# Kernel tuning notes

Measured on AMD Instinct MI355X. Metric: run time of the kernel, lower is better.

Reference implementation:

```python
import jax, jax.numpy as jnp
import numpy as np

N_NODES = 20000
N_EDGES = 50000
IN_DIM = 128
HID = 128
OUT_DIM = 64
N_PAIRS = 128
N_LAYERS = 2
N_HEADS = 4


def setup_inputs() -> dict:
    key = jax.random.key(0)
    ks = jax.random.split(key, 32)
    s = 0.05
    def p(k, shape):
        return jax.random.normal(k, shape, jnp.float32) * s
    inp = {}
    inp["node_features"] = jax.random.normal(ks[0], (N_NODES, IN_DIM), jnp.float32)
    inp["edge_index"] = jax.random.randint(ks[1], (2, N_EDGES), 0, N_NODES, jnp.int32)
    inp["edge_timestamps"] = jax.random.uniform(ks[2], (N_EDGES,), jnp.float32)
    inp["target_pairs"] = jax.random.randint(ks[3], (N_PAIRS, 2), 0, N_NODES, jnp.int32)
    inp["in_W"] = p(ks[4], (HID, IN_DIM)); inp["in_b"] = p(ks[5], (HID,))
    inp["te_W1"] = p(ks[6], (N_LAYERS, HID, 1)); inp["te_b1"] = p(ks[7], (N_LAYERS, HID))
    inp["te_W2"] = p(ks[8], (N_LAYERS, HID, HID)); inp["te_b2"] = p(ks[9], (N_LAYERS, HID))
    inp["attn_in_W"] = p(ks[10], (N_LAYERS, 3 * HID, HID)); inp["attn_in_b"] = p(ks[11], (N_LAYERS, 3 * HID))
    inp["attn_out_W"] = p(ks[12], (N_LAYERS, HID, HID)); inp["attn_out_b"] = p(ks[13], (N_LAYERS, HID))
    inp["ft_W"] = p(ks[14], (N_LAYERS, HID, HID)); inp["ft_b"] = p(ks[15], (N_LAYERS, HID))
    inp["op_W"] = p(ks[16], (N_LAYERS, HID, HID)); inp["op_b"] = p(ks[17], (N_LAYERS, HID))
    inp["out1_W"] = p(ks[18], (HID, HID)); inp["out1_b"] = p(ks[19], (HID,))
    inp["out2_W"] = p(ks[20], (OUT_DIM, HID)); inp["out2_b"] = p(ks[21], (OUT_DIM,))
    inp["lp1_W"] = p(ks[22], (HID, 2 * OUT_DIM)); inp["lp1_b"] = p(ks[23], (HID,))
    inp["lp2_W"] = p(ks[24], (HID // 2, HID)); inp["lp2_b"] = p(ks[25], (HID // 2,))
    inp["lp3_W"] = p(ks[26], (1, HID // 2)); inp["lp3_b"] = p(ks[27], (1,))
    return inp


def _forward(node_features, edge_index, edge_timestamps, target_pairs,
             in_W, in_b, te_W1, te_b1, te_W2, te_b2,
             attn_in_W, attn_in_b, attn_out_W, attn_out_b,
             ft_W, ft_b, op_W, op_b,
             out1_W, out1_b, out2_W, out2_b,
             lp1_W, lp1_b, lp2_W, lp2_b, lp3_W, lp3_b):
    N = node_features.shape[0]
    h = in_W.shape[0]
    H = N_HEADS
    d = h // H
    scale = 1.0 / np.sqrt(d).astype(np.float32)
    src, dst = edge_index[0], edge_index[1]
    # flattened target nodes; duplicates compute identical rows so dedup (torch.unique) is unneeded
    targets = target_pairs.reshape(-1)  # [U]
    U = targets.shape[0]
    E = src.shape[0]

    x = node_features @ in_W.T + in_b  # [N, h]
    for l in range(te_W1.shape[0]):
        tf = x @ ft_W[l].T + ft_b[l]                                           # [N, h]
        tfeat = jax.nn.relu(edge_timestamps[:, None] @ te_W1[l].T + te_b1[l])
        tfeat = tfeat @ te_W2[l].T + te_b2[l]                                  # [E, h]
        Wq, Wk, Wv = jnp.split(attn_in_W[l], 3, axis=0)
        bq, bk, bv = jnp.split(attn_in_b[l], 3)
        q = (tf[targets] @ Wq.T + bq).reshape(U, H, d)
        # keys/values are linear in (tf[nbr] + tfeat): split into node term A and edge term B
        Ak = (tf @ Wk.T).reshape(N, H, d)
        Bk = (tfeat @ Wk.T + bk).reshape(E, H, d)
        Av = (tf @ Wv.T).reshape(N, H, d)
        Bv = (tfeat @ Wv.T + bv).reshape(E, H, d)
        is_src = src[None, :] == targets[:, None]          # [U, E]
        mask = is_src | (dst[None, :] == targets[:, None])  # edge incident to target
        nbr = jnp.where(is_src, dst[None, :], src[None, :])  # other endpoint, [U, E]
        qAk = jnp.einsum('uhd,nhd->uhn', q, Ak) * scale      # [U, H, N]
        idx = jnp.broadcast_to(nbr[:, None, :], (U, H, E))
        s_node = jnp.take_along_axis(qAk, idx, axis=2)        # [U, H, E]
        s_edge = jnp.einsum('uhd,ehd->uhe', q, Bk) * scale
        scores = jnp.where(mask[:, None, :], s_node + s_edge, -1e30)
        p = jax.nn.softmax(scores, axis=-1)
        p = jnp.where(mask[:, None, :], p, 0.0)               # [U, H, E]
        out_edge = jnp.einsum('uhe,ehd->uhd', p, Bv)
        # sum_e p * Av[nbr] via per-target scatter of probs into node space
        w = jax.vmap(lambda pe, ne: jax.ops.segment_sum(pe, ne, num_segments=N))(
            p.transpose(0, 2, 1), nbr)                        # [U, N, H]
        out_node = jnp.einsum('unh,nhd->uhd', w, Av)
        attn = (out_node + out_edge).reshape(U, h) @ attn_out_W[l].T + attn_out_b[l]
        has_nbr = mask.any(axis=1)
        agg_in = jnp.where(has_nbr[:, None], attn, tf[targets])
        agg = agg_in @ op_W[l].T + op_b[l]
        x = x.at[targets].set(agg)
        x = jax.nn.relu(x)
    emb = jax.nn.relu(x @ out1_W.T + out1_b) @ out2_W.T + out2_b  # [N, out]
    pair = jnp.concatenate([emb[target_pairs[:, 0]], emb[target_pairs[:, 1]]], axis=1)
    z = jax.nn.relu(pair @ lp1_W.T + lp1_b)
    z = jax.nn.relu(z @ lp2_W.T + lp2_b)
    return jax.nn.sigmoid(z @ lp3_W.T + lp3_b)  # [B, 1]


def reference(node_features, edge_index, edge_timestamps, target_pairs,
              in_W, in_b, te_W1, te_b1, te_W2, te_b2,
              attn_in_W, attn_in_b, attn_out_W, attn_out_b,
              ft_W, ft_b, op_W, op_b,
              out1_W, out1_b, out2_W, out2_b,
              lp1_W, lp1_b, lp2_W, lp2_b, lp3_W, lp3_b):
    return _forward(node_features, edge_index, edge_timestamps, target_pairs,
                    in_W, in_b, te_W1, te_b1, te_W2, te_b2,
                    attn_in_W, attn_in_b, attn_out_W, attn_out_b,
                    ft_W, ft_b, op_W, op_b,
                    out1_W, out1_b, out2_W, out2_b,
                    lp1_W, lp1_b, lp2_W, lp2_b, lp3_W, lp3_b)
```

## Files before the change

kernel.cpp:

```cpp
#include <hip/hip_runtime.h>
#include <math.h>

#define N_NODES 20000
#define N_EDGES 50000
#define N_SLOTS 256
#define N_PAIRS 128
#define CAP 32
#define MSTRIDE 16384
#define NMAT 19
#define TFLAG (1 << 30)
#define HSZ 1024
#define NBLK 256

__device__ __forceinline__ float4 relu4(float4 v) {
    return make_float4(fmaxf(v.x, 0.f), fmaxf(v.y, 0.f), fmaxf(v.z, 0.f), fmaxf(v.w, 0.f));
}
__device__ __forceinline__ float4 add4(float4 a, float4 b) {
    return make_float4(a.x + b.x, a.y + b.y, a.z + b.z, a.w + b.w);
}
__device__ __forceinline__ void fma4(float4& acc, const float4 w, const float s) {
    acc.x = fmaf(w.x, s, acc.x); acc.y = fmaf(w.y, s, acc.y);
    acc.z = fmaf(w.z, s, acc.z); acc.w = fmaf(w.w, s, acc.w);
}
#define F4Z make_float4(0.f, 0.f, 0.f, 0.f)

__device__ __forceinline__ void gbar(unsigned* cnt, unsigned target, bool wait) {
    __syncthreads();
    if (threadIdx.x == 0) {
        __builtin_amdgcn_fence(__ATOMIC_RELEASE, "agent");
        __hip_atomic_fetch_add(cnt, 1u, __ATOMIC_RELAXED, __HIP_MEMORY_SCOPE_AGENT);
        if (wait) {
            int it = 0;
            while (true) {
                unsigned v;
                if ((it++ & 7) != 7)
                    v = __hip_atomic_load(cnt, __ATOMIC_RELAXED,
                                          __HIP_MEMORY_SCOPE_SYSTEM);
                else
                    v = __hip_atomic_fetch_add(cnt, 0u, __ATOMIC_RELAXED,
                                               __HIP_MEMORY_SCOPE_AGENT);
                if (v >= target) break;
                __builtin_amdgcn_s_sleep(16);
            }
            __builtin_amdgcn_fence(__ATOMIC_ACQUIRE, "agent");
        }
    }
    __syncthreads();
}

__device__ __forceinline__ float4 mv_ks1_g8(const float* __restrict__ WT,
                                            const float* __restrict__ xv128,
                                            int g, int jj) {
    const float4* W4 = (const float4*)WT;
    const float4* x4 = (const float4*)xv128;
    float4 acc = F4Z;
#pragma unroll
    for (int kk4 = 0; kk4 < 4; ++kk4) {
        int k4 = g * 4 + kk4;
        float4 xv = x4[k4];
        fma4(acc, W4[(k4 * 4 + 0) * 32 + jj], xv.x);
        fma4(acc, W4[(k4 * 4 + 1) * 32 + jj], xv.y);
        fma4(acc, W4[(k4 * 4 + 2) * 32 + jj], xv.z);
        fma4(acc, W4[(k4 * 4 + 3) * 32 + jj], xv.w);
    }
    return acc;
}
__device__ __forceinline__ float4 mv_ks1_g8_64(const float* __restrict__ WT,
                                               const float* __restrict__ xv128,
                                               int g, int jj) {
    const float4* W4 = (const float4*)WT;
    const float4* x4 = (const float4*)xv128;
    int j16 = jj & 15;
    float4 acc = F4Z;
#pragma unroll
    for (int kk4 = 0; kk4 < 4; ++kk4) {
        int k4 = g * 4 + kk4;
        float4 xv = x4[k4];
        fma4(acc, W4[(k4 * 4 + 0) * 16 + j16], xv.x);
        fma4(acc, W4[(k4 * 4 + 1) * 16 + j16], xv.y);
        fma4(acc, W4[(k4 * 4 + 2) * 16 + j16], xv.z);
        fma4(acc, W4[(k4 * 4 + 3) * 16 + j16], xv.w);
    }
    return acc;
}
__device__ __forceinline__ void mv8_g8(const float* __restrict__ WT,
                                       const float* __restrict__ xs,
                                       int g, int jj, float4* acc) {
    const float4* W4 = (const float4*)WT;
    const float4* x4 = (const float4*)xs;
#pragma unroll
    for (int kk4 = 0; kk4 < 4; ++kk4) {
        int k4 = g * 4 + kk4;
        float4 w0 = W4[(k4 * 4 + 0) * 32 + jj];
        float4 w1 = W4[(k4 * 4 + 1) * 32 + jj];
        float4 w2 = W4[(k4 * 4 + 2) * 32 + jj];
        float4 w3 = W4[(k4 * 4 + 3) * 32 + jj];
#pragma unroll
        for (int e = 0; e < 8; ++e) {
            float4 xv = x4[e * 32 + k4];
            fma4(acc[e], w0, xv.x); fma4(acc[e], w1, xv.y);
            fma4(acc[e], w2, xv.z); fma4(acc[e], w3, xv.w);
        }
    }
}
__device__ __forceinline__ float4 comb1_g8(const float4* pb, int jj) {
    float4 s = pb[jj];
#pragma unroll
    for (int gp = 1; gp < 8; ++gp) s = add4(s, pb[gp * 32 + jj]);
    return s;
}
__device__ __forceinline__ float4 comb8_g8(const float4* pb, int it, int jj) {
    float4 s = pb[it * 32 + jj];
#pragma unroll
    for (int gp = 1; gp < 8; ++gp) s = add4(s, pb[(gp * 8 + it) * 32 + jj]);
    return s;
}

__device__ __forceinline__ float4 mv_ks1(const float* __restrict__ WT,
                                         const float* __restrict__ xv128,
                                         int g, int jj) {
    const float4* W4 = (const float4*)WT;
    const float4* x4 = (const float4*)xv128;
    float4 acc = F4Z;
#pragma unroll 2
    for (int kk4 = 0; kk4 < 8; ++kk4) {
        int k4 = g * 8 + kk4;
        float4 xv = x4[k4];
        fma4(acc, W4[(k4 * 4 + 0) * 32 + jj], xv.x);
        fma4(acc, W4[(k4 * 4 + 1) * 32 + jj], xv.y);
        fma4(acc, W4[(k4 * 4 + 2) * 32 + jj], xv.z);
        fma4(acc, W4[(k4 * 4 + 3) * 32 + jj], xv.w);
    }
    return acc;
}
__device__ __forceinline__ float4 mv_ks1_64(const float* __restrict__ WT,
                                            const float* __restrict__ xv128,
                                            int g, int jj) {
    const float4* W4 = (const float4*)WT;
    const float4* x4 = (const float4*)xv128;
    int j16 = jj & 15;
    float4 acc = F4Z;
#pragma unroll 2
    for (int kk4 = 0; kk4 < 8; ++kk4) {
        int k4 = g * 8 + kk4;
        float4 xv = x4[k4];
        fma4(acc, W4[(k4 * 4 + 0) * 16 + j16], xv.x);
        fma4(acc, W4[(k4 * 4 + 1) * 16 + j16], xv.y);
        fma4(acc, W4[(k4 * 4 + 2) * 16 + j16], xv.z);
        fma4(acc, W4[(k4 * 4 + 3) * 16 + j16], xv.w);
    }
    return acc;
}
__device__ __forceinline__ float4 comb1(const float4* pb, int jj) {
    return add4(add4(pb[jj], pb[32 + jj]), add4(pb[64 + jj], pb[96 + jj]));
}

__device__ __forceinline__ unsigned thash(int key) {
    return ((unsigned)key * 2654435761u) >> 22;
}
__device__ __forceinline__ bool hexists(const int* __restrict__ hkey, int key) {
    unsigned h = thash(key);
    while (true) {
        int k = hkey[h];
        if (k == -1) return false;
        if (k == key) return true;
        h = (h + 1) & (HSZ - 1);
    }
}
__device__ __forceinline__ void hemit_g(const int* __restrict__ hkey,
                                        const int* __restrict__ hval,
                                        int* __restrict__ gcnt,
                                        int2* __restrict__ lst,
                                        int key, int e, int nbrf) {
    unsigned h = thash(key);
    while (true) {
        int k = hkey[h];
        if (k == -1) return;
        if (k == key) {
            int s = hval[h];
            int pos = atomicAdd(&gcnt[s], 1);
            if (pos < CAP) lst[s * CAP + pos] = make_int2(e, nbrf);
        }
        h = (h + 1) & (HSZ - 1);
    }
}

struct Params {
    const float* nf; const int* ei; const float* ts; const int* tp;
    const float* inW; const float* inb;
    const float* teW1; const float* teb1; const float* teW2; const float* teb2;
    const float* aiW; const float* aib; const float* aoW; const float* aob;
    const float* ftW; const float* ftb; const float* opW; const float* opb;
    const float* o1W; const float* o1b; const float* o2W; const float* o2b;
    const float* l1W; const float* l1b; const float* l2W; const float* l2b;
    const float* l3W; const float* l3b;
    float* out; float* x; int* cnt; int2* lst; float* emb; float* WT;
    unsigned* bar;
};

__global__ __launch_bounds__(256, 1) void k_fused(Params P) {
    __shared__ __align__(16) float xu[128], x0u[128], tfv[128], qv[128], sv[128];
    __shared__ __align__(16) float xs[8 * 128], t1s[8 * 128], x0s[8 * 128], zs[8 * 128];
    __shared__ __align__(16) float4 pb[8 * 8 * 32];
    __shared__ __align__(16) float vbl[CAP * 128];
    __shared__ float scl[CAP * 4];
    __shared__ int nbr_s[8], tf_s[8];
    __shared__ float ts_s[8];
    __shared__ __align__(16) float tile[32][129];
    __shared__ int hkey[HSZ], hval[HSZ];

    const int b = blockIdx.x, tid = threadIdx.x, g = tid >> 5, jj = tid & 31;

    if (b < 72) {
        int m, r0, rows;
        if (b < 68) { m = b >> 2; r0 = (b & 3) * 32; rows = 128; }
        else { int mm = b - 68; m = 17 + (mm >> 1); r0 = (mm & 1) * 32; rows = 64; }
        const float* src;
        if (m == 0) src = P.inW;
        else if (m <= 2) src = P.ftW + (m - 1) * MSTRIDE;
        else if (m <= 4) src = P.teW2 + (m - 3) * MSTRIDE;
        else if (m <= 10) src = P.aiW + (m - 5) * MSTRIDE;
        else if (m <= 12) src = P.aoW + (m - 11) * MSTRIDE;
        else if (m <= 14) src = P.opW + (m - 13) * MSTRIDE;
        else if (m == 15) src = P.o1W;
        else if (m == 16) src = P.l1W;
        else if (m == 17) src = P.o2W;
        else src = P.l2W;
        float* dst = P.WT + m * MSTRIDE;
        for (int idx = tid; idx < 32 * 128; idx += 256) {
            int r = idx >> 7, cc = idx & 127;
            tile[r][cc] = src[(r0 + r) * 128 + cc];
        }
        __syncthreads();
        for (int idx = tid; idx < 128 * 32; idx += 256) {
            int k = idx >> 5, jr = idx & 31;
            dst[k * rows + r0 + jr] = tile[jr][k];
        }
    } else {
        for (int i = tid; i < HSZ; i += 256) hkey[i] = -1;
        __syncthreads();
        {
            int uu = P.tp[tid];
            unsigned h = thash(uu);
            while (atomicCAS(&hkey[h], -1, uu) != -1) h = (h + 1) & (HSZ - 1);
            hval[h] = tid;
        }
        __syncthreads();
        const int4* s4 = (const int4*)P.ei;
        const int4* d4 = (const int4*)(P.ei + N_EDGES);
        const int NE4 = N_EDGES / 4;
        const int nscan = NBLK - 72;
        const int chunk = (NE4 + nscan - 1) / nscan;
        const int start = (b - 72) * chunk;
        const int end = min(start + chunk, NE4);
        for (int e4 = start + tid; e4 < end; e4 += 256) {
            int4 s = s4[e4];
            int4 d = d4[e4];
            int ss[4] = {s.x, s.y, s.z, s.w};
            int dd[4] = {d.x, d.y, d.z, d.w};
#pragma unroll
            for (int t = 0; t < 4; ++t) {
                int a = ss[t], bb = dd[t];
                bool atgt = hexists(hkey, a);
                bool btgt = (bb == a) ? atgt : hexists(hkey, bb);
                if (!atgt && !btgt) continue;
                int e = e4 * 4 + t;
                if (atgt) hemit_g(hkey, hval, P.cnt, P.lst, a, e, bb | (btgt ? TFLAG : 0));
                if (btgt && bb != a) hemit_g(hkey, hval, P.cnt, P.lst, bb, e, a | (atgt ? TFLAG : 0));
            }
        }
    }
    gbar(P.bar, NBLK, true);

    const float scale = 0.17677669529663687f;
    const int u = P.tp[b];
    const int c = min(P.cnt[b], CAP);

    for (int layer = 0; layer < 2; ++layer) {
        const float* WT_in = P.WT;
        const float* WT_ft = P.WT + (1 + layer) * MSTRIDE;
        const float* WT_te2 = P.WT + (3 + layer) * MSTRIDE;
        const float* WT_q = P.WT + (5 + 3 * layer) * MSTRIDE;
        const float* WT_k = P.WT + (6 + 3 * layer) * MSTRIDE;
        const float* WT_v = P.WT + (7 + 3 * layer) * MSTRIDE;
        const float* WT_ao = P.WT + (11 + layer) * MSTRIDE;
        const float* WT_op = P.WT + (13 + layer) * MSTRIDE;
        const float* inb = P.inb;
        const float* ftb = P.ftb + layer * 128;
        const float* teW1 = P.teW1 + layer * 128;
        const float* teb1 = P.teb1 + layer * 128;
        const float* teb2 = P.teb2 + layer * 128;
        const float* bq = P.aib + layer * 384;
        const float* bk = bq + 128;
        const float* bv = bq + 256;
        const float* aob = P.aob + layer * 128;
        const float* opb = P.opb + layer * 128;

        if (tid < 128) xu[tid] = (layer == 0) ? P.nf[(size_t)u * 128 + tid]
                                              : P.x[(size_t)u * 128 + tid];
        __syncthreads();
        const float* xeff = xu;
        if (layer == 0) {
            pb[g * 32 + jj] = mv_ks1_g8(WT_in, xu, g, jj);
            __syncthreads();
            if (g == 0)
                *(float4*)(x0u + jj * 4) = add4(comb1_g8(pb, jj), *(const float4*)(inb + jj * 4));
            xeff = x0u;
            __syncthreads();
        }
        pb[g * 32 + jj] = mv_ks1_g8(WT_ft, xeff, g, jj);
        __syncthreads();
        if (g == 0)
            *(float4*)(tfv + jj * 4) = add4(comb1_g8(pb, jj), *(const float4*)(ftb + jj * 4));
        __syncthreads();
        pb[g * 32 + jj] = mv_ks1_g8(WT_q, tfv, g, jj);
        __syncthreads();
        if (g == 0)
            *(float4*)(qv + jj * 4) = add4(comb1_g8(pb, jj), *(const float4*)(bq + jj * 4));
        __syncthreads();

        for (int base = 0; base < c; base += 8) {
            if (tid < 8) {
                int i = base + tid;
                int2 en = (i < c) ? P.lst[b * CAP + i] : make_int2(0, 0);
                nbr_s[tid] = en.y & ~TFLAG;
                tf_s[tid] = (en.y & TFLAG) ? 1 : 0;
                ts_s[tid] = (i < c) ? P.ts[en.x] : 0.f;
            }
            __syncthreads();
            {
                int e = tid >> 5, c0 = jj * 4;
                const float* srcp = (layer == 0) ? (P.nf + (size_t)nbr_s[e] * 128 + c0)
                                                 : (P.x + (size_t)nbr_s[e] * 128 + c0);
                float4 v = *(const float4*)srcp;
                float* dstp = (layer == 0) ? xs : x0s;
                *(float4*)(dstp + e * 128 + c0) = v;
                float tse = ts_s[e];
                float4 w = *(const float4*)(teW1 + c0);
                float4 bb = *(const float4*)(teb1 + c0);
                *(float4*)(t1s + e * 128 + c0) =
                    make_float4(fmaxf(fmaf(tse, w.x, bb.x), 0.f),
                                fmaxf(fmaf(tse, w.y, bb.y), 0.f),
                                fmaxf(fmaf(tse, w.z, bb.z), 0.f),
                                fmaxf(fmaf(tse, w.w, bb.w), 0.f));
            }
            __syncthreads();
            if (layer == 0) {
                float4 acc[8] = {F4Z, F4Z, F4Z, F4Z, F4Z, F4Z, F4Z, F4Z};
                mv8_g8(WT_in, xs, g, jj, acc);
#pragma unroll
                for (int e = 0; e < 8; ++e) pb[(g * 8 + e) * 32 + jj] = acc[e];
                __syncthreads();
                {
                    float4 x0v = add4(comb8_g8(pb, g, jj), *(const float4*)(inb + jj * 4));
                    *(float4*)(x0s + g * 128 + jj * 4) = x0v;
                    if (base + g < c && !tf_s[g])
                        *(float4*)(P.x + (size_t)nbr_s[g] * 128 + jj * 4) = relu4(x0v);
                }
                __syncthreads();
            }
            {
                float4 acc[8] = {F4Z, F4Z, F4Z, F4Z, F4Z, F4Z, F4Z, F4Z};
                mv8_g8(WT_ft, x0s, g, jj, acc);
#pragma unroll
                for (int e = 0; e < 8; ++e) pb[(g * 8 + e) * 32 + jj] = acc[e];
                __syncthreads();
                float4 za = comb8_g8(pb, g, jj);
                __syncthreads();
                float4 acc2[8] = {F4Z, F4Z, F4Z, F4Z, F4Z, F4Z, F4Z, F4Z};
                mv8_g8(WT_te2, t1s, g, jj, acc2);
#pragma unroll
                for (int e = 0; e < 8; ++e) pb[(g * 8 + e) * 32 + jj] = acc2[e];
                __syncthreads();
                float4 zb = comb8_g8(pb, g, jj);
                float4 z4 = add4(add4(za, zb),
                                 add4(*(const float4*)(ftb + jj * 4),
                                      *(const float4*)(teb2 + jj * 4)));
                *(float4*)(zs + g * 128 + jj * 4) = z4;
                __syncthreads();
            }
            {
                float4 acc[8] = {F4Z, F4Z, F4Z, F4Z, F4Z, F4Z, F4Z, F4Z};
                mv8_g8(WT_k, zs, g, jj, acc);
#pragma unroll
                for (int e = 0; e < 8; ++e) pb[(g * 8 + e) * 32 + jj] = acc[e];
                __syncthreads();
                float4 kk = add4(comb8_g8(pb, g, jj), *(const float4*)(bk + jj * 4));
                __syncthreads();
                float4 acc2[8] = {F4Z, F4Z, F4Z, F4Z, F4Z, F4Z, F4Z, F4Z};
                mv8_g8(WT_v, zs, g, jj, acc2);
#pragma unroll
                for (int e = 0; e < 8; ++e) pb[(g * 8 + e) * 32 + jj] = acc2[e];
                __syncthreads();
                float4 vv = add4(comb8_g8(pb, g, jj), *(const float4*)(bv + jj * 4));
                float4 q4 = *(const float4*)(qv + jj * 4);
                float pr = q4.x * kk.x + q4.y * kk.y + q4.z * kk.z + q4.w * kk.w;
                pr += __shfl_xor(pr, 1);
                pr += __shfl_xor(pr, 2);
                pr += __shfl_xor(pr, 4);
                if (base + g < c) {
                    if ((jj & 7) == 0) scl[(base + g) * 4 + (jj >> 3)] = pr * scale;
                    *(float4*)(vbl + (base + g) * 128 + jj * 4) = vv;
                }
                __syncthreads();
            }
        }

        if (tid < 128) {
            int h = tid >> 5;
            if (c > 0) {
                float m = -INFINITY;
                for (int i = 0; i < c; ++i) m = fmaxf(m, scl[i * 4 + h]);
                float l = 0.f, o = 0.f;
                for (int i = 0; i < c; ++i) {
                    float p = __expf(scl[i * 4 + h] - m);
                    l += p;
                    o = fmaf(p, vbl[i * 128 + tid], o);
                }
                sv[tid] = o / l;
            } else {
                sv[tid] = 0.f;
            }
        }
        __syncthreads();
        pb[g * 32 + jj] = mv_ks1_g8(WT_ao, sv, g, jj);
        __syncthreads();
        if (g == 0) {
            float4 z4;
            if (c > 0) z4 = add4(comb1_g8(pb, jj), *(const float4*)(aob + jj * 4));
            else z4 = *(const float4*)(tfv + jj * 4);
            *(float4*)(xu + jj * 4) = z4;
        }
        __syncthreads();
        pb[g * 32 + jj] = mv_ks1_g8(WT_op, xu, g, jj);
        __syncthreads();
        if (layer == 0) {
            if (g == 0) {
                float4 a = relu4(add4(comb1_g8(pb, jj), *(const float4*)(opb + jj * 4)));
                *(float4*)(P.x + (size_t)u * 128 + jj * 4) = a;
            }
        } else {
            if (g == 0)
                *(float4*)(x0u + jj * 4) =
                    relu4(add4(comb1_g8(pb, jj), *(const float4*)(opb + jj * 4)));
            __syncthreads();
            pb[g * 32 + jj] = mv_ks1_g8(P.WT + 15 * MSTRIDE, x0u, g, jj);
            __syncthreads();
            if (g == 0)
                *(float4*)(tfv + jj * 4) =
                    relu4(add4(comb1_g8(pb, jj), *(const float4*)(P.o1b + jj * 4)));
            __syncthreads();
            pb[g * 32 + jj] = mv_ks1_g8_64(P.WT + 17 * MSTRIDE, tfv, g, jj);
            __syncthreads();
            if (g == 0 && jj < 16)
                *(float4*)(P.emb + (size_t)b * 64 + jj * 4) =
                    add4(comb1_g8(pb, jj), *(const float4*)(P.o2b + jj * 4));
        }
        gbar(P.bar, NBLK * (2 + layer), layer == 0 || b < N_PAIRS);
    }

    if (b < N_PAIRS) {
        const float* WT_l1 = P.WT + 16 * MSTRIDE;
        const float* WT_l2 = P.WT + 18 * MSTRIDE;
        if (tid < 128)
            xu[tid] = (tid < 64) ? P.emb[(size_t)(2 * b) * 64 + tid]
                                 : P.emb[(size_t)(2 * b + 1) * 64 + (tid - 64)];
        __syncthreads();
        if (tid < 128) pb[g * 32 + jj] = mv_ks1(WT_l1, xu, g, jj);
        __syncthreads();
        if (tid < 128 && g == 0)
            *(float4*)(tfv + jj * 4) =
                relu4(add4(comb1(pb, jj), *(const float4*)(P.l1b + jj * 4)));
        __syncthreads();
        if (tid < 128) pb[g * 32 + jj] = mv_ks1_64(WT_l2, tfv, g, jj);
        __syncthreads();
        if (tid < 128 && g == 0 && jj < 16)
            *(float4*)(qv + jj * 4) =
                relu4(add4(comb1(pb, jj), *(const float4*)(P.l2b + jj * 4)));
        __syncthreads();
        if (tid < 64) {
            float v = qv[tid] * P.l3W[tid];
            v += __shfl_xor(v, 1);
            v += __shfl_xor(v, 2);
            v += __shfl_xor(v, 4);
            v += __shfl_xor(v, 8);
            v += __shfl_xor(v, 16);
            v += __shfl_xor(v, 32);
            if (tid == 0) P.out[b] = 1.f / (1.f + __expf(-(v + P.l3b[0])));
        }
    }
}

extern "C" void kernel_launch(void* const* d_in, const int* in_sizes, int n_in,
                              void* d_out, int out_size, void* d_ws, size_t ws_size,
                              hipStream_t stream) {
    Params P;
    P.nf  = (const float*)d_in[0];
    P.ei  = (const int*)d_in[1];
    P.ts  = (const float*)d_in[2];
    P.tp  = (const int*)d_in[3];
    P.inW = (const float*)d_in[4];
    P.inb = (const float*)d_in[5];
    P.teW1 = (const float*)d_in[6];
    P.teb1 = (const float*)d_in[7];
    P.teW2 = (const float*)d_in[8];
    P.teb2 = (const float*)d_in[9];
    P.aiW = (const float*)d_in[10];
    P.aib = (const float*)d_in[11];
    P.aoW = (const float*)d_in[12];
    P.aob = (const float*)d_in[13];
    P.ftW = (const float*)d_in[14];
    P.ftb = (const float*)d_in[15];
    P.opW = (const float*)d_in[16];
    P.opb = (const float*)d_in[17];
    P.o1W = (const float*)d_in[18];
    P.o1b = (const float*)d_in[19];
    P.o2W = (const float*)d_in[20];
    P.o2b = (const float*)d_in[21];
    P.l1W = (const float*)d_in[22];
    P.l1b = (const float*)d_in[23];
    P.l2W = (const float*)d_in[24];
    P.l2b = (const float*)d_in[25];
    P.l3W = (const float*)d_in[26];
    P.l3b = (const float*)d_in[27];
    P.out = (float*)d_out;

    char* ws = (char*)d_ws;
    size_t off = 0;
    P.x    = (float*)(ws + off); off += (size_t)N_NODES * 128 * 4;
    P.cnt  = (int*)  (ws + off); off += N_SLOTS * 4;
    P.lst  = (int2*) (ws + off); off += (size_t)N_SLOTS * CAP * 8;
    P.emb  = (float*)(ws + off); off += N_SLOTS * 64 * 4;
    P.WT   = (float*)(ws + off); off += (size_t)NMAT * MSTRIDE * 4;
    P.bar  = (unsigned*)(ws + off); off += 256;

    hipMemsetAsync(P.cnt, 0, N_SLOTS * 4, stream);
    hipMemsetAsync(P.bar, 0, 4, stream);
    k_fused<<<NBLK, 256, 0, stream>>>(P);
}
```

Baseline: 205.3 us.

## Double block size to 512 threads and process 16 neighbors per batch

```diff
diff --git a/kernel.cpp b/kernel.cpp
--- a/kernel.cpp
+++ b/kernel.cpp
@@ -11,6 +11,8 @@
 #define TFLAG (1 << 30)
 #define HSZ 1024
 #define NBLK 256
+#define NTHR 512
+#define BATCH 16
 
 __device__ __forceinline__ float4 relu4(float4 v) {
     return make_float4(fmaxf(v.x, 0.f), fmaxf(v.y, 0.f), fmaxf(v.z, 0.f), fmaxf(v.w, 0.f));
@@ -48,15 +50,15 @@
     __syncthreads();
 }
 
-__device__ __forceinline__ float4 mv_ks1_g8(const float* __restrict__ WT,
-                                            const float* __restrict__ xv128,
-                                            int g, int jj) {
+__device__ __forceinline__ float4 mv_ks1_g16(const float* __restrict__ WT,
+                                             const float* __restrict__ xv128,
+                                             int gall, int jj) {
     const float4* W4 = (const float4*)WT;
     const float4* x4 = (const float4*)xv128;
     float4 acc = F4Z;
 #pragma unroll
-    for (int kk4 = 0; kk4 < 4; ++kk4) {
-        int k4 = g * 4 + kk4;
+    for (int kk4 = 0; kk4 < 2; ++kk4) {
+        int k4 = gall * 2 + kk4;
         float4 xv = x4[k4];
         fma4(acc, W4[(k4 * 4 + 0) * 32 + jj], xv.x);
         fma4(acc, W4[(k4 * 4 + 1) * 32 + jj], xv.y);
@@ -65,16 +67,16 @@
     }
     return acc;
 }
-__device__ __forceinline__ float4 mv_ks1_g8_64(const float* __restrict__ WT,
-                                               const float* __restrict__ xv128,
-                                               int g, int jj) {
+__device__ __forceinline__ float4 mv_ks1_g16_64(const float* __restrict__ WT,
+                                                const float* __restrict__ xv128,
+                                                int gall, int jj) {
     const float4* W4 = (const float4*)WT;
     const float4* x4 = (const float4*)xv128;
     int j16 = jj & 15;
     float4 acc = F4Z;
 #pragma unroll
-    for (int kk4 = 0; kk4 < 4; ++kk4) {
-        int k4 = g * 4 + kk4;
+    for (int kk4 = 0; kk4 < 2; ++kk4) {
+        int k4 = gall * 2 + kk4;
         float4 xv = x4[k4];
         fma4(acc, W4[(k4 * 4 + 0) * 16 + j16], xv.x);
         fma4(acc, W4[(k4 * 4 + 1) * 16 + j16], xv.y);
@@ -83,6 +85,13 @@
     }
     return acc;
 }
+__device__ __forceinline__ float4 comb1_g16(const float4* pb, int jj) {
+    float4 s = pb[jj];
+#pragma unroll
+    for (int gp = 1; gp < 16; ++gp) s = add4(s, pb[gp * 32 + jj]);
+    return s;
+}
+
 __device__ __forceinline__ void mv8_g8(const float* __restrict__ WT,
                                        const float* __restrict__ xs,
                                        int g, int jj, float4* acc) {
@@ -102,12 +111,6 @@
             fma4(acc[e], w2, xv.z); fma4(acc[e], w3, xv.w);
         }
     }
-}
-__device__ __forceinline__ float4 comb1_g8(const float4* pb, int jj) {
-    float4 s = pb[jj];
-#pragma unroll
-    for (int gp = 1; gp < 8; ++gp) s = add4(s, pb[gp * 32 + jj]);
-    return s;
 }
 __device__ __forceinline__ float4 comb8_g8(const float4* pb, int it, int jj) {
     float4 s = pb[it * 32 + jj];
@@ -198,18 +201,21 @@
     unsigned* bar;
 };
 
-__global__ __launch_bounds__(256, 1) void k_fused(Params P) {
+__global__ __launch_bounds__(NTHR, 1) void k_fused(Params P) {
     __shared__ __align__(16) float xu[128], x0u[128], tfv[128], qv[128], sv[128];
-    __shared__ __align__(16) float xs[8 * 128], t1s[8 * 128], x0s[8 * 128], zs[8 * 128];
-    __shared__ __align__(16) float4 pb[8 * 8 * 32];
+    __shared__ __align__(16) float xs[BATCH * 128], t1s[BATCH * 128];
+    __shared__ __align__(16) float x0s[BATCH * 128], zs[BATCH * 128];
+    __shared__ __align__(16) float4 pb[2 * 8 * 8 * 32];
     __shared__ __align__(16) float vbl[CAP * 128];
     __shared__ float scl[CAP * 4];
-    __shared__ int nbr_s[8], tf_s[8];
-    __shared__ float ts_s[8];
+    __shared__ int nbr_s[BATCH], tf_s[BATCH];
+    __shared__ float ts_s[BATCH];
     __shared__ __align__(16) float tile[32][129];
     __shared__ int hkey[HSZ], hval[HSZ];
 
-    const int b = blockIdx.x, tid = threadIdx.x, g = tid >> 5, jj = tid & 31;
+    const int b = blockIdx.x, tid = threadIdx.x;
+    const int jj = tid & 31, gall = tid >> 5;
+    const int h = gall >> 3, g = gall & 7;
 
     if (b < 72) {
         int m, r0, rows;
@@ -227,23 +233,23 @@
         else if (m == 17) src = P.o2W;
         else src = P.l2W;
         float* dst = P.WT + m * MSTRIDE;
-        for (int idx = tid; idx < 32 * 128; idx += 256) {
+        for (int idx = tid; idx < 32 * 128; idx += NTHR) {
             int r = idx >> 7, cc = idx & 127;
             tile[r][cc] = src[(r0 + r) * 128 + cc];
         }
         __syncthreads();
-        for (int idx = tid; idx < 128 * 32; idx += 256) {
+        for (int idx = tid; idx < 128 * 32; idx += NTHR) {
             int k = idx >> 5, jr = idx & 31;
             dst[k * rows + r0 + jr] = tile[jr][k];
         }
     } else {
-        for (int i = tid; i < HSZ; i += 256) hkey[i] = -1;
-        __syncthreads();
-        {
+        for (int i = tid; i < HSZ; i += NTHR) hkey[i] = -1;
+        __syncthreads();
+        if (tid < N_SLOTS) {
             int uu = P.tp[tid];
-            unsigned h = thash(uu);
-            while (atomicCAS(&hkey[h], -1, uu) != -1) h = (h + 1) & (HSZ - 1);
-            hval[h] = tid;
+            unsigned hh = thash(uu);
+            while (atomicCAS(&hkey[hh], -1, uu) != -1) hh = (hh + 1) & (HSZ - 1);
+            hval[hh] = tid;
         }
         __syncthreads();
         const int4* s4 = (const int4*)P.ei;
@@ -253,7 +259,7 @@
         const int chunk = (NE4 + nscan - 1) / nscan;
         const int start = (b - 72) * chunk;
         const int end = min(start + chunk, NE4);
-        for (int e4 = start + tid; e4 < end; e4 += 256) {
+        for (int e4 = start + tid; e4 < end; e4 += NTHR) {
             int4 s = s4[e4];
             int4 d = d4[e4];
             int ss[4] = {s.x, s.y, s.z, s.w};
@@ -301,26 +307,26 @@
         __syncthreads();
         const float* xeff = xu;
         if (layer == 0) {
-            pb[g * 32 + jj] = mv_ks1_g8(WT_in, xu, g, jj);
-            __syncthreads();
-            if (g == 0)
-                *(float4*)(x0u + jj * 4) = add4(comb1_g8(pb, jj), *(const float4*)(inb + jj * 4));
+            pb[gall * 32 + jj] = mv_ks1_g16(WT_in, xu, gall, jj);
+            __syncthreads();
+            if (gall == 0)
+                *(float4*)(x0u + jj * 4) = add4(comb1_g16(pb, jj), *(const float4*)(inb + jj * 4));
             xeff = x0u;
             __syncthreads();
         }
-        pb[g * 32 + jj] = mv_ks1_g8(WT_ft, xeff, g, jj);
-        __syncthreads();
-        if (g == 0)
-            *(float4*)(tfv + jj * 4) = add4(comb1_g8(pb, jj), *(const float4*)(ftb + jj * 4));
-        __syncthreads();
-        pb[g * 32 + jj] = mv_ks1_g8(WT_q, tfv, g, jj);
-        __syncthreads();
-        if (g == 0)
-            *(float4*)(qv + jj * 4) = add4(comb1_g8(pb, jj), *(const float4*)(bq + jj * 4));
-        __syncthreads();
-
-        for (int base = 0; base < c; base += 8) {
-            if (tid < 8) {
+        pb[gall * 32 + jj] = mv_ks1_g16(WT_ft, xeff, gall, jj);
+        __syncthreads();
+        if (gall == 0)
+            *(float4*)(tfv + jj * 4) = add4(comb1_g16(pb, jj), *(const float4*)(ftb + jj * 4));
+        __syncthreads();
+        pb[gall * 32 + jj] = mv_ks1_g16(WT_q, tfv, gall, jj);
+        __syncthreads();
+        if (gall == 0)
+            *(float4*)(qv + jj * 4) = add4(comb1_g16(pb, jj), *(const float4*)(bq + jj * 4));
+        __syncthreads();
+
+        for (int base = 0; base < c; base += BATCH) {
+            if (tid < BATCH) {
                 int i = base + tid;
                 int2 en = (i < c) ? P.lst[b * CAP + i] : make_int2(0, 0);
                 nbr_s[tid] = en.y & ~TFLAG;
@@ -329,7 +335,7 @@
             }
             __syncthreads();
             {
-                int e = tid >> 5, c0 = jj * 4;
+                int e = gall, c0 = jj * 4;
                 const float* srcp = (layer == 0) ? (P.nf + (size_t)nbr_s[e] * 128 + c0)
                                                  : (P.x + (size_t)nbr_s[e] * 128 + c0);
                 float4 v = *(const float4*)srcp;
@@ -345,75 +351,81 @@
                                 fmaxf(fmaf(tse, w.w, bb.w), 0.f));
             }
             __syncthreads();
+            float4* pbh = pb + h * (8 * 8 * 32);
+            const float* xsh = xs + h * 8 * 128;
+            const float* x0sh = x0s + h * 8 * 128;
+            const float* t1sh = t1s + h * 8 * 128;
+            const float* zsh = zs + h * 8 * 128;
+            const int item = base + h * 8 + g;
             if (layer == 0) {
                 float4 acc[8] = {F4Z, F4Z, F4Z, F4Z, F4Z, F4Z, F4Z, F4Z};
-                mv8_g8(WT_in, xs, g, jj, acc);
-#pragma unroll
-                for (int e = 0; e < 8; ++e) pb[(g * 8 + e) * 32 + jj] = acc[e];
+                mv8_g8(WT_in, xsh, g, jj, acc);
+#pragma unroll
+                for (int e = 0; e < 8; ++e) pbh[(g * 8 + e) * 32 + jj] = acc[e];
                 __syncthreads();
                 {
-                    float4 x0v = add4(comb8_g8(pb, g, jj), *(const float4*)(inb + jj * 4));
-                    *(float4*)(x0s + g * 128 + jj * 4) = x0v;
-                    if (base + g < c && !tf_s[g])
-                        *(float4*)(P.x + (size_t)nbr_s[g] * 128 + jj * 4) = relu4(x0v);
+                    float4 x0v = add4(comb8_g8(pbh, g, jj), *(const float4*)(inb + jj * 4));
+                    *(float4*)(x0s + (h * 8 + g) * 128 + jj * 4) = x0v;
+                    if (item < c && !tf_s[h * 8 + g])
+                        *(float4*)(P.x + (size_t)nbr_s[h * 8 + g] * 128 + jj * 4) = relu4(x0v);
                 }
                 __syncthreads();
             }
             {
                 float4 acc[8] = {F4Z, F4Z, F4Z, F4Z, F4Z, F4Z, F4Z, F4Z};
-                mv8_g8(WT_ft, x0s, g, jj, acc);
-#pragma unroll
-                for (int e = 0; e < 8; ++e) pb[(g * 8 + e) * 32 + jj] = acc[e];
-                __syncthreads();
-                float4 za = comb8_g8(pb, g, jj);
+                mv8_g8(WT_ft, x0sh, g, jj, acc);
+#pragma unroll
+                for (int e = 0; e < 8; ++e) pbh[(g * 8 + e) * 32 + jj] = acc[e];
+                __syncthreads();
+                float4 za = comb8_g8(pbh, g, jj);
                 __syncthreads();
                 float4 acc2[8] = {F4Z, F4Z, F4Z, F4Z, F4Z, F4Z, F4Z, F4Z};
-                mv8_g8(WT_te2, t1s, g, jj, acc2);
-#pragma unroll
-                for (int e = 0; e < 8; ++e) pb[(g * 8 + e) * 32 + jj] = acc2[e];
-                __syncthreads();
-                float4 zb = comb8_g8(pb, g, jj);
+                mv8_g8(WT_te2, t1sh, g, jj, acc2);
+#pragma unroll
+                for (int e = 0; e < 8; ++e) pbh[(g * 8 + e) * 32 + jj] = acc2[e];
+                __syncthreads();
+                float4 zb = comb8_g8(pbh, g, jj);
                 float4 z4 = add4(add4(za, zb),
                                  add4(*(const float4*)(ftb + jj * 4),
                                       *(const float4*)(teb2 + jj * 4)));
-                *(float4*)(zs + g * 128 + jj * 4) = z4;
+                *(float4*)(zs + (h * 8 + g) * 128 + jj * 4) = z4;
                 __syncthreads();
             }
             {
                 float4 acc[8] = {F4Z, F4Z, F4Z, F4Z, F4Z, F4Z, F4Z, F4Z};
-                mv8_g8(WT_k, zs, g, jj, acc);
-#pragma unroll
-                for (int e = 0; e < 8; ++e) pb[(g * 8 + e) * 32 + jj] = acc[e];
-                __syncthreads();
-                float4 kk = add4(comb8_g8(pb, g, jj), *(const float4*)(bk + jj * 4));
+                mv8_g8(WT_k, zsh, g, jj, acc);
+#pragma unroll
+                for (int e = 0; e < 8; ++e) pbh[(g * 8 + e) * 32 + jj] = acc[e];
+                __syncthreads();
+                float4 kk = add4(comb8_g8(pbh, g, jj), *(const float4*)(bk + jj * 4));
                 __syncthreads();
                 float4 acc2[8] = {F4Z, F4Z, F4Z, F4Z, F4Z, F4Z, F4Z, F4Z};
-                mv8_g8(WT_v, zs, g, jj, acc2);
-#pragma unroll
-                for (int e = 0; e < 8; ++e) pb[(g * 8 + e) * 32 + jj] = acc2[e];
-                __syncthreads();
-                float4 vv = add4(comb8_g8(pb, g, jj), *(const float4*)(bv + jj * 4));
+                mv8_g8(WT_v, zsh, g, jj, acc2);
+#pragma unroll
+                for (int e = 0; e < 8; ++e) pbh[(g * 8 + e) * 32 + jj] = acc2[e];
+                __syncthreads();
+                float4 vv = add4(comb8_g8(pbh, g, jj), *(const float4*)(bv + jj * 4));
                 float4 q4 = *(const float4*)(qv + jj * 4);
                 float pr = q4.x * kk.x + q4.y * kk.y + q4.z * kk.z + q4.w * kk.w;
                 pr += __shfl_xor(pr, 1);
                 pr += __shfl_xor(pr, 2);
                 pr += __shfl_xor(pr, 4);
-                if (base + g < c) {
-                    if ((jj & 7) == 0) scl[(base + g) * 4 + (jj >> 3)] = pr * scale;
-                    *(float4*)(vbl + (base + g) * 128 + jj * 4) = vv;
+                if (item < c) {
+                    if ((jj & 7) == 0) scl[item * 4 + (jj >> 3)] = pr * scale;
+                    *(float4*)(vbl + item * 128 + jj * 4) = vv;
                 }
                 __syncthreads();
             }
         }
 
         if (tid < 128) {
-            int h = tid >> 5;
+            int hd = tid >> 5;
             if (c > 0) {
                 float m = -INFINITY;
-                for (int i = 0; i < c; ++i) m = fmaxf(m, scl[i * 4 + h]);
+                for (int i = 0; i < c; ++i) m = fmaxf(m, scl[i * 4 + hd]);
                 float l = 0.f, o = 0.f;
                 for (int i = 0; i < c; ++i) {
-                    float p = __expf(scl[i * 4 + h] - m);
+                    float p = __expf(scl[i * 4 + hd] - m);
                     l += p;
                     o = fmaf(p, vbl[i * 128 + tid], o);
                 }
@@ -423,38 +435,38 @@
             }
         }
         __syncthreads();
-        pb[g * 32 + jj] = mv_ks1_g8(WT_ao, sv, g, jj);
-        __syncthreads();
-        if (g == 0) {
+        pb[gall * 32 + jj] = mv_ks1_g16(WT_ao, sv, gall, jj);
+        __syncthreads();
+        if (gall == 0) {
             float4 z4;
-            if (c > 0) z4 = add4(comb1_g8(pb, jj), *(const float4*)(aob + jj * 4));
+            if (c > 0) z4 = add4(comb1_g16(pb, jj), *(const float4*)(aob + jj * 4));
             else z4 = *(const float4*)(tfv + jj * 4);
             *(float4*)(xu + jj * 4) = z4;
         }
         __syncthreads();
-        pb[g * 32 + jj] = mv_ks1_g8(WT_op, xu, g, jj);
+        pb[gall * 32 + jj] = mv_ks1_g16(WT_op, xu, gall, jj);
         __syncthreads();
         if (layer == 0) {
-            if (g == 0) {
-                float4 a = relu4(add4(comb1_g8(pb, jj), *(const float4*)(opb + jj * 4)));
+            if (gall == 0) {
+                float4 a = relu4(add4(comb1_g16(pb, jj), *(const float4*)(opb + jj * 4)));
                 *(float4*)(P.x + (size_t)u * 128 + jj * 4) = a;
             }
         } else {
-            if (g == 0)
+            if (gall == 0)
                 *(float4*)(x0u + jj * 4) =
-                    relu4(add4(comb1_g8(pb, jj), *(const float4*)(opb + jj * 4)));
-            __syncthreads();
-            pb[g * 32 + jj] = mv_ks1_g8(P.WT + 15 * MSTRIDE, x0u, g, jj);
-            __syncthreads();
-            if (g == 0)
+                    relu4(add4(comb1_g16(pb, jj), *(const float4*)(opb + jj * 4)));
+            __syncthreads();
+            pb[gall * 32 + jj] = mv_ks1_g16(P.WT + 15 * MSTRIDE, x0u, gall, jj);
+            __syncthreads();
+            if (gall == 0)
                 *(float4*)(tfv + jj * 4) =
-                    relu4(add4(comb1_g8(pb, jj), *(const float4*)(P.o1b + jj * 4)));
-            __syncthreads();
-            pb[g * 32 + jj] = mv_ks1_g8_64(P.WT + 17 * MSTRIDE, tfv, g, jj);
-            __syncthreads();
-            if (g == 0 && jj < 16)
+                    relu4(add4(comb1_g16(pb, jj), *(const float4*)(P.o1b + jj * 4)));
+            __syncthreads();
+            pb[gall * 32 + jj] = mv_ks1_g16_64(P.WT + 17 * MSTRIDE, tfv, gall, jj);
+            __syncthreads();
+            if (gall == 0 && jj < 16)
                 *(float4*)(P.emb + (size_t)b * 64 + jj * 4) =
-                    add4(comb1_g8(pb, jj), *(const float4*)(P.o2b + jj * 4));
+                    add4(comb1_g16(pb, jj), *(const float4*)(P.o2b + jj * 4));
         }
         gbar(P.bar, NBLK * (2 + layer), layer == 0 || b < N_PAIRS);
     }
@@ -466,15 +478,15 @@
             xu[tid] = (tid < 64) ? P.emb[(size_t)(2 * b) * 64 + tid]
                                  : P.emb[(size_t)(2 * b + 1) * 64 + (tid - 64)];
         __syncthreads();
-        if (tid < 128) pb[g * 32 + jj] = mv_ks1(WT_l1, xu, g, jj);
-        __syncthreads();
-        if (tid < 128 && g == 0)
+        if (tid < 128) pb[gall * 32 + jj] = mv_ks1(WT_l1, xu, gall, jj);
+        __syncthreads();
+        if (tid < 128 && gall == 0)
             *(float4*)(tfv + jj * 4) =
                 relu4(add4(comb1(pb, jj), *(const float4*)(P.l1b + jj * 4)));
         __syncthreads();
-        if (tid < 128) pb[g * 32 + jj] = mv_ks1_64(WT_l2, tfv, g, jj);
-        __syncthreads();
-        if (tid < 128 && g == 0 && jj < 16)
+        if (tid < 128) pb[gall * 32 + jj] = mv_ks1_64(WT_l2, tfv, gall, jj);
+        __syncthreads();
+        if (tid < 128 && gall == 0 && jj < 16)
             *(float4*)(qv + jj * 4) =
                 relu4(add4(comb1(pb, jj), *(const float4*)(P.l2b + jj * 4)));
         __syncthreads();
@@ -536,5 +548,5 @@
 
     hipMemsetAsync(P.cnt, 0, N_SLOTS * 4, stream);
     hipMemsetAsync(P.bar, 0, 4, stream);
-    k_fused<<<NBLK, 256, 0, stream>>>(P);
-}
+    k_fused<<<NBLK, NTHR, 0, stream>>>(P);
+}
```

Result: slower. 239.6 us (+16.7%).

## Batch neighbor processing in groups of 16 and fuse ft/te2 matvecs

Applied to the files above, without the earlier changes.

```diff
diff --git a/kernel.cpp b/kernel.cpp
--- a/kernel.cpp
+++ b/kernel.cpp
@@ -11,6 +11,7 @@
 #define TFLAG (1 << 30)
 #define HSZ 1024
 #define NBLK 256
+#define BATCH 16
 
 __device__ __forceinline__ float4 relu4(float4 v) {
     return make_float4(fmaxf(v.x, 0.f), fmaxf(v.y, 0.f), fmaxf(v.z, 0.f), fmaxf(v.w, 0.f));
@@ -83,9 +84,16 @@
     }
     return acc;
 }
-__device__ __forceinline__ void mv8_g8(const float* __restrict__ WT,
-                                       const float* __restrict__ xs,
-                                       int g, int jj, float4* acc) {
+__device__ __forceinline__ float4 comb1_g8(const float4* pb, int jj) {
+    float4 s = pb[jj];
+#pragma unroll
+    for (int gp = 1; gp < 8; ++gp) s = add4(s, pb[gp * 32 + jj]);
+    return s;
+}
+
+__device__ __forceinline__ void mv16_g8(const float* __restrict__ WT,
+                                        const float* __restrict__ xs,
+                                        int g, int jj, float4* acc) {
     const float4* W4 = (const float4*)WT;
     const float4* x4 = (const float4*)xs;
 #pragma unroll
@@ -96,23 +104,17 @@
         float4 w2 = W4[(k4 * 4 + 2) * 32 + jj];
         float4 w3 = W4[(k4 * 4 + 3) * 32 + jj];
 #pragma unroll
-        for (int e = 0; e < 8; ++e) {
+        for (int e = 0; e < 16; ++e) {
             float4 xv = x4[e * 32 + k4];
             fma4(acc[e], w0, xv.x); fma4(acc[e], w1, xv.y);
             fma4(acc[e], w2, xv.z); fma4(acc[e], w3, xv.w);
         }
     }
 }
-__device__ __forceinline__ float4 comb1_g8(const float4* pb, int jj) {
-    float4 s = pb[jj];
-#pragma unroll
-    for (int gp = 1; gp < 8; ++gp) s = add4(s, pb[gp * 32 + jj]);
-    return s;
-}
-__device__ __forceinline__ float4 comb8_g8(const float4* pb, int it, int jj) {
+__device__ __forceinline__ float4 comb16_g8(const float4* pb, int it, int jj) {
     float4 s = pb[it * 32 + jj];
 #pragma unroll
-    for (int gp = 1; gp < 8; ++gp) s = add4(s, pb[(gp * 8 + it) * 32 + jj]);
+    for (int gp = 1; gp < 8; ++gp) s = add4(s, pb[(gp * 16 + it) * 32 + jj]);
     return s;
 }
 
@@ -200,12 +202,13 @@
 
 __global__ __launch_bounds__(256, 1) void k_fused(Params P) {
     __shared__ __align__(16) float xu[128], x0u[128], tfv[128], qv[128], sv[128];
-    __shared__ __align__(16) float xs[8 * 128], t1s[8 * 128], x0s[8 * 128], zs[8 * 128];
-    __shared__ __align__(16) float4 pb[8 * 8 * 32];
+    __shared__ __align__(16) float xs[BATCH * 128], t1s[BATCH * 128];
+    __shared__ __align__(16) float x0s[BATCH * 128], zs[BATCH * 128];
+    __shared__ __align__(16) float4 pb[8 * 16 * 32];
     __shared__ __align__(16) float vbl[CAP * 128];
     __shared__ float scl[CAP * 4];
-    __shared__ int nbr_s[8], tf_s[8];
-    __shared__ float ts_s[8];
+    __shared__ int nbr_s[BATCH], tf_s[BATCH];
+    __shared__ float ts_s[BATCH];
     __shared__ __align__(16) float tile[32][129];
     __shared__ int hkey[HSZ], hval[HSZ];
 
@@ -319,8 +322,8 @@
             *(float4*)(qv + jj * 4) = add4(comb1_g8(pb, jj), *(const float4*)(bq + jj * 4));
         __syncthreads();
 
-        for (int base = 0; base < c; base += 8) {
-            if (tid < 8) {
+        for (int base = 0; base < c; base += BATCH) {
+            if (tid < BATCH) {
                 int i = base + tid;
                 int2 en = (i < c) ? P.lst[b * CAP + i] : make_int2(0, 0);
                 nbr_s[tid] = en.y & ~TFLAG;
@@ -329,91 +332,107 @@
             }
             __syncthreads();
             {
-                int e = tid >> 5, c0 = jj * 4;
-                const float* srcp = (layer == 0) ? (P.nf + (size_t)nbr_s[e] * 128 + c0)
-                                                 : (P.x + (size_t)nbr_s[e] * 128 + c0);
-                float4 v = *(const float4*)srcp;
-                float* dstp = (layer == 0) ? xs : x0s;
-                *(float4*)(dstp + e * 128 + c0) = v;
-                float tse = ts_s[e];
+                int c0 = jj * 4;
                 float4 w = *(const float4*)(teW1 + c0);
                 float4 bb = *(const float4*)(teb1 + c0);
-                *(float4*)(t1s + e * 128 + c0) =
-                    make_float4(fmaxf(fmaf(tse, w.x, bb.x), 0.f),
-                                fmaxf(fmaf(tse, w.y, bb.y), 0.f),
-                                fmaxf(fmaf(tse, w.z, bb.z), 0.f),
-                                fmaxf(fmaf(tse, w.w, bb.w), 0.f));
+#pragma unroll
+                for (int s = 0; s < 2; ++s) {
+                    int e = g + s * 8;
+                    const float* srcp = (layer == 0) ? (P.nf + (size_t)nbr_s[e] * 128 + c0)
+                                                     : (P.x + (size_t)nbr_s[e] * 128 + c0);
+                    float4 v = *(const float4*)srcp;
+                    float* dstp = (layer == 0) ? xs : x0s;
+                    *(float4*)(dstp + e * 128 + c0) = v;
+                    float tse = ts_s[e];
+                    *(float4*)(t1s + e * 128 + c0) =
+                        make_float4(fmaxf(fmaf(tse, w.x, bb.x), 0.f),
+                                    fmaxf(fmaf(tse, w.y, bb.y), 0.f),
+                                    fmaxf(fmaf(tse, w.z, bb.z), 0.f),
+                                    fmaxf(fmaf(tse, w.w, bb.w), 0.f));
+                }
             }
             __syncthreads();
             if (layer == 0) {
-                float4 acc[8] = {F4Z, F4Z, F4Z, F4Z, F4Z, F4Z, F4Z, F4Z};
-                mv8_g8(WT_in, xs, g, jj, acc);
-#pragma unroll
-                for (int e = 0; e < 8; ++e) pb[(g * 8 + e) * 32 + jj] = acc[e];
-                __syncthreads();
-                {
-                    float4 x0v = add4(comb8_g8(pb, g, jj), *(const float4*)(inb + jj * 4));
-                    *(float4*)(x0s + g * 128 + jj * 4) = x0v;
-                    if (base + g < c && !tf_s[g])
-                        *(float4*)(P.x + (size_t)nbr_s[g] * 128 + jj * 4) = relu4(x0v);
+                float4 acc[16] = {F4Z, F4Z, F4Z, F4Z, F4Z, F4Z, F4Z, F4Z,
+                                  F4Z, F4Z, F4Z, F4Z, F4Z, F4Z, F4Z, F4Z};
+                mv16_g8(WT_in, xs, g, jj, acc);
+#pragma unroll
+                for (int e = 0; e < 16; ++e) pb[(g * 16 + e) * 32 + jj] = acc[e];
+                __syncthreads();
+#pragma unroll
+                for (int s = 0; s < 2; ++s) {
+                    int it = 2 * g + s;
+                    float4 x0v = add4(comb16_g8(pb, it, jj), *(const float4*)(inb + jj * 4));
+                    *(float4*)(x0s + it * 128 + jj * 4) = x0v;
+                    if (base + it < c && !tf_s[it])
+                        *(float4*)(P.x + (size_t)nbr_s[it] * 128 + jj * 4) = relu4(x0v);
                 }
                 __syncthreads();
             }
             {
-                float4 acc[8] = {F4Z, F4Z, F4Z, F4Z, F4Z, F4Z, F4Z, F4Z};
-                mv8_g8(WT_ft, x0s, g, jj, acc);
-#pragma unroll
-                for (int e = 0; e < 8; ++e) pb[(g * 8 + e) * 32 + jj] = acc[e];
-                __syncthreads();
-                float4 za = comb8_g8(pb, g, jj);
-                __syncthreads();
-                float4 acc2[8] = {F4Z, F4Z, F4Z, F4Z, F4Z, F4Z, F4Z, F4Z};
-                mv8_g8(WT_te2, t1s, g, jj, acc2);
-#pragma unroll
-                for (int e = 0; e < 8; ++e) pb[(g * 8 + e) * 32 + jj] = acc2[e];
-                __syncthreads();
-                float4 zb = comb8_g8(pb, g, jj);
-                float4 z4 = add4(add4(za, zb),
-                                 add4(*(const float4*)(ftb + jj * 4),
-                                      *(const float4*)(teb2 + jj * 4)));
-                *(float4*)(zs + g * 128 + jj * 4) = z4;
+                float4 acc[16] = {F4Z, F4Z, F4Z, F4Z, F4Z, F4Z, F4Z, F4Z,
+                                  F4Z, F4Z, F4Z, F4Z, F4Z, F4Z, F4Z, F4Z};
+                mv16_g8(WT_ft, x0s, g, jj, acc);
+                mv16_g8(WT_te2, t1s, g, jj, acc);
+#pragma unroll
+                for (int e = 0; e < 16; ++e) pb[(g * 16 + e) * 32 + jj] = acc[e];
+                __syncthreads();
+                float4 zb4 = add4(*(const float4*)(ftb + jj * 4),
+                                  *(const float4*)(teb2 + jj * 4));
+#pragma unroll
+                for (int s = 0; s < 2; ++s) {
+                    int it = 2 * g + s;
+                    *(float4*)(zs + it * 128 + jj * 4) = add4(comb16_g8(pb, it, jj), zb4);
+                }
                 __syncthreads();
             }
             {
-                float4 acc[8] = {F4Z, F4Z, F4Z, F4Z, F4Z, F4Z, F4Z, F4Z};
-                mv8_g8(WT_k, zs, g, jj, acc);
-#pragma unroll
-                for (int e = 0; e < 8; ++e) pb[(g * 8 + e) * 32 + jj] = acc[e];
-                __syncthreads();
-                float4 kk = add4(comb8_g8(pb, g, jj), *(const float4*)(bk + jj * 4));
-                __syncthreads();
-                float4 acc2[8] = {F4Z, F4Z, F4Z, F4Z, F4Z, F4Z, F4Z, F4Z};
-                mv8_g8(WT_v, zs, g, jj, acc2);
-#pragma unroll
-                for (int e = 0; e < 8; ++e) pb[(g * 8 + e) * 32 + jj] = acc2[e];
-                __syncthreads();
-                float4 vv = add4(comb8_g8(pb, g, jj), *(const float4*)(bv + jj * 4));
+                float4 acc[16] = {F4Z, F4Z, F4Z, F4Z, F4Z, F4Z, F4Z, F4Z,
+                                  F4Z, F4Z, F4Z, F4Z, F4Z, F4Z, F4Z, F4Z};
+                mv16_g8(WT_k, zs, g, jj, acc);
+#pragma unroll
+                for (int e = 0; e < 16; ++e) pb[(g * 16 + e) * 32 + jj] = acc[e];
+                __syncthreads();
                 float4 q4 = *(const float4*)(qv + jj * 4);
-                float pr = q4.x * kk.x + q4.y * kk.y + q4.z * kk.z + q4.w * kk.w;
-                pr += __shfl_xor(pr, 1);
-                pr += __shfl_xor(pr, 2);
-                pr += __shfl_xor(pr, 4);
-                if (base + g < c) {
-                    if ((jj & 7) == 0) scl[(base + g) * 4 + (jj >> 3)] = pr * scale;
-                    *(float4*)(vbl + (base + g) * 128 + jj * 4) = vv;
+#pragma unroll
+                for (int s = 0; s < 2; ++s) {
+                    int it = 2 * g + s;
+                    float4 kk = add4(comb16_g8(pb, it, jj), *(const float4*)(bk + jj * 4));
+                    float pr = q4.x * kk.x + q4.y * kk.y + q4.z * kk.z + q4.w * kk.w;
+                    pr += __shfl_xor(pr, 1);
+                    pr += __shfl_xor(pr, 2);
+                    pr += __shfl_xor(pr, 4);
+                    if (base + it < c && (jj & 7) == 0)
+                        scl[(base + it) * 4 + (jj >> 3)] = pr * scale;
                 }
                 __syncthreads();
             }
+            {
+                float4 acc[16] = {F4Z, F4Z, F4Z, F4Z, F4Z, F4Z, F4Z, F4Z,
+                                  F4Z, F4Z, F4Z, F4Z, F4Z, F4Z, F4Z, F4Z};
+                mv16_g8(WT_v, zs, g, jj, acc);
+#pragma unroll
+                for (int e = 0; e < 16; ++e) pb[(g * 16 + e) * 32 + jj] = acc[e];
+                __syncthreads();
+#pragma unroll
+                for (int s = 0; s < 2; ++s) {
+                    int it = 2 * g + s;
+                    float4 vv = add4(comb16_g8(pb, it, jj), *(const float4*)(bv + jj * 4));
+                    if (base + it < c)
+                        *(float4*)(vbl + (base + it) * 128 + jj * 4) = vv;
+                }
+                __syncthreads();
+            }
         }
 
         if (tid < 128) {
-            int h = tid >> 5;
+            int hd = tid >> 5;
             if (c > 0) {
                 float m = -INFINITY;
-                for (int i = 0; i < c; ++i) m = fmaxf(m, scl[i * 4 + h]);
+                for (int i = 0; i < c; ++i) m = fmaxf(m, scl[i * 4 + hd]);
                 float l = 0.f, o = 0.f;
                 for (int i = 0; i < c; ++i) {
-                    float p = __expf(scl[i * 4 + h] - m);
+                    float p = __expf(scl[i * 4 + hd] - m);
                     l += p;
                     o = fmaf(p, vbl[i * 128 + tid], o);
                 }
```

New measurement: 196.5 us. 4.3% less time.
